# Optimization experiments

Measured on AMD Instinct MI355X. Metric: run time of the kernel, lower is better.

## Reference

```python
import jax, jax.numpy as jnp
import numpy as np

H, D, E, C, F = 12, 64, 768, 512, 3072  # heads, kq_dim, emb_dim, context_dim, mlp_hid
EPS = 1e-5
SCALE = 1.0 / float(np.sqrt(D))


def setup_inputs() -> dict:
    key = jax.random.key(0)
    ks = jax.random.split(key, 12)
    rn = lambda k, s: jax.random.normal(k, s, dtype=jnp.float32) * 0.02
    z = lambda s: jnp.zeros(s, jnp.float32)
    o = lambda s: jnp.ones(s, jnp.float32)
    return {
        "emb": jax.random.normal(ks[0], (8, 1024, E), dtype=jnp.float32),
        "context": jax.random.normal(ks[1], (8, 256, C), dtype=jnp.float32),
        # self-attention (qkv_bias=False, value_up has bias)
        "sa_wq": rn(ks[2], (E, H * D)), "sa_wk": rn(ks[3], (E, H * D)),
        "sa_wv": rn(ks[4], (E, H * D)), "sa_wo": rn(ks[5], (H * D, E)), "sa_wo_b": z((E,)),
        "sa_qn_g": o((D,)), "sa_qn_b": z((D,)), "sa_kn_g": o((D,)), "sa_kn_b": z((D,)),
        # cross-attention
        "ca_wq": rn(ks[6], (E, H * D)), "ca_wk": rn(ks[7], (C, H * D)),
        "ca_wv": rn(ks[8], (C, H * D)), "ca_wo": rn(ks[9], (H * D, E)), "ca_wo_b": z((E,)),
        "ca_qn_g": o((D,)), "ca_qn_b": z((D,)), "ca_kn_g": o((D,)), "ca_kn_b": z((D,)),
        # MLP
        "mlp_w1": rn(ks[10], (E, F)), "mlp_b1": z((F,)),
        "mlp_w2": rn(ks[11], (F, E)), "mlp_b2": z((E,)),
        # block LayerNorms
        "ln1_g": o((E,)), "ln1_b": z((E,)),
        "ln2_g": o((E,)), "ln2_b": z((E,)),
        "ln3_g": o((E,)), "ln3_b": z((E,)),
    }


def _ln(x, g, b):
    m = jnp.mean(x, axis=-1, keepdims=True)
    v = jnp.mean(jnp.square(x - m), axis=-1, keepdims=True)
    return (x - m) / jnp.sqrt(v + EPS) * g + b


def _heads(x):  # [B,S,H*D] -> [B,H,S,D]
    B, S = x.shape[:2]
    return x.reshape(B, S, H, D).transpose(0, 2, 1, 3)


def _merge(x):  # [B,H,S,D] -> [B,S,H*D]
    B, h, S, d = x.shape
    return x.transpose(0, 2, 1, 3).reshape(B, S, h * d)


def _attn(qx, kvx, wq, wk, wv, wo, wo_b, qg, qb, kg, kb):
    q = _ln(_heads(qx @ wq), qg, qb)   # per-head QK-LayerNorm
    k = _ln(_heads(kvx @ wk), kg, kb)
    v = _heads(kvx @ wv)
    a = jax.nn.softmax(jnp.einsum('bhqd,bhkd->bhqk', q, k) * SCALE, axis=-1)
    return _merge(jnp.einsum('bhqk,bhkd->bhqd', a, v)) @ wo + wo_b


def reference(emb, context,
              sa_wq, sa_wk, sa_wv, sa_wo, sa_wo_b, sa_qn_g, sa_qn_b, sa_kn_g, sa_kn_b,
              ca_wq, ca_wk, ca_wv, ca_wo, ca_wo_b, ca_qn_g, ca_qn_b, ca_kn_g, ca_kn_b,
              mlp_w1, mlp_b1, mlp_w2, mlp_b2,
              ln1_g, ln1_b, ln2_g, ln2_b, ln3_g, ln3_b):
    # MultiHeadAttention.forward returns value + emb, and the block adds emb again
    sa = _attn(emb, emb, sa_wq, sa_wk, sa_wv, sa_wo, sa_wo_b,
               sa_qn_g, sa_qn_b, sa_kn_g, sa_kn_b)
    x = _ln(sa + emb + emb, ln1_g, ln1_b)  # faithful double residual
    ca = _attn(x, context, ca_wq, ca_wk, ca_wv, ca_wo, ca_wo_b,
               ca_qn_g, ca_qn_b, ca_kn_g, ca_kn_b)
    x = _ln(x + ca, ln2_g, ln2_b)
    x = jax.nn.gelu(x @ mlp_w1 + mlp_b1, approximate=False) @ mlp_w2 + mlp_b2
    return _ln(x, ln3_g, ln3_b)  # note: no residual around MLP in the original
```

## Files before the change

kernel.cpp:

```cpp
#include <hip/hip_runtime.h>
#include <hip/hip_bf16.h>
#include <math.h>

#define NH 12
#define HD 64
#define ED 768
#define CD 512
#define FD 3072
#define BB 8
#define SS 1024
#define TT 256
#define LN_EPS 1e-5f
#define ATT_SCALE 0.125f
#define QSC_LOG2E 0.1803368801111204f
#define P_M0 11.55f
#define TOT_R 6291456

typedef __attribute__((ext_vector_type(8))) __bf16 bf16x8;
typedef __attribute__((ext_vector_type(4))) __bf16 bf16x4;
typedef __attribute__((ext_vector_type(4))) float f32x4;

typedef const __attribute__((address_space(1))) void* gas1_t;
typedef __attribute__((address_space(3))) void* las3_t;

__device__ __forceinline__ void gl16(const void* g, void* l) {
  __builtin_amdgcn_global_load_lds((gas1_t)g, (las3_t)l, 16, 0, 0);
}

__device__ __forceinline__ ushort f2bf(float f) {
  union { __bf16 b; ushort u; } c;
  c.b = (__bf16)f;
  return c.u;
}

__device__ __forceinline__ float gelu_fast(float c) {
  const float x2 = c * c;
  const float ex = __builtin_amdgcn_exp2f(c * (-2.3022084f - 0.10294325f * x2));
  return c * __builtin_amdgcn_rcpf(1.0f + ex);
}

__device__ __forceinline__ bf16x8 frag64(const ushort (*T)[64], int row, int q8) {
  return *(const bf16x8*)((const char*)T + row * 128 + ((q8 ^ (row & 7)) << 4));
}

__device__ __forceinline__ bf16x8 frag32(const ushort (*T)[32], int row, int g) {
  return *(const bf16x8*)((const char*)T + row * 64 + ((g ^ ((row >> 1) & 3)) << 4));
}

struct CvtPack {
  const float* src[12];
  ushort* dst[12];
  int kd[12];
  int nd[12];
  int off[13];
};

__global__ __launch_bounds__(256) void cvt_all(CvtPack P) {
  __shared__ float t[32][33];
  const int flat = blockIdx.x;
  int j = 0;
  while (j < 11 && flat >= P.off[j + 1]) ++j;
  const int rel = flat - P.off[j];
  if (P.nd[j] == 0) {
    const int i = rel * 256 + threadIdx.x;
    if (i < P.kd[j]) {
      float4 v = ((const float4*)P.src[j])[i];
      ((ushort4*)P.dst[j])[i] =
          make_ushort4(f2bf(v.x), f2bf(v.y), f2bf(v.z), f2bf(v.w));
    }
    return;
  }
  const int Kd = P.kd[j], Nd = P.nd[j];
  const int ntx = Nd >> 5;
  const int n0 = (rel % ntx) * 32, k0 = (rel / ntx) * 32;
  const float* W = P.src[j];
  ushort* WT = P.dst[j];
  const int tx = threadIdx.x & 31, ty = threadIdx.x >> 5;
#pragma unroll
  for (int r = 0; r < 4; ++r)
    t[ty + 8 * r][tx] = W[(size_t)(k0 + ty + 8 * r) * Nd + n0 + tx];
  __syncthreads();
#pragma unroll
  for (int r = 0; r < 4; ++r)
    WT[(size_t)(n0 + ty + 8 * r) * Kd + k0 + tx] = f2bf(t[tx][ty + 8 * r]);
}

template <int MODE, int BM>
__global__ __launch_bounds__(256, 3) void mfma_gemm(
    const ushort* __restrict__ A, const ushort* __restrict__ Wt,
    const float* __restrict__ bias, void* __restrict__ outp,
    int M, int N, int K, int sshift,
    const float* __restrict__ qg, const float* __restrict__ qb,
    const float* __restrict__ kg, const float* __restrict__ kb,
    int t_q, int t_k, int t_v) {
  constexpr int MI = BM / 32;
  __shared__ ushort As[2][BM][32];
  __shared__ ushort Bs[2][128][32];
  const int tid = threadIdx.x;
  const int m0 = blockIdx.x * BM, n0 = blockIdx.y * 128;
  const int lane = tid & 63;
  const int wr = ((tid >> 6) >> 1) * (BM / 2), wc = ((tid >> 6) & 1) * 64;
  const int l15 = lane & 15, g = lane >> 4;
  f32x4 acc[MI][4] = {};

  auto stage = [&](int bi, int kt) {
#pragma unroll
    for (int p = 0; p < BM / 64; ++p) {
      const int fq = p * 256 + tid;
      const int row = fq >> 2, q = fq & 3;
      const int kc = 8 * (q ^ ((row >> 1) & 3));
      gl16(&A[(size_t)(m0 + row) * K + kt + kc], (char*)As[bi] + fq * 16);
    }
#pragma unroll
    for (int p = 0; p < 2; ++p) {
      const int fq = p * 256 + tid;
      const int row = fq >> 2, q = fq & 3;
      const int kc = 8 * (q ^ ((row >> 1) & 3));
      gl16(&Wt[(size_t)(n0 + row) * K + kt + kc], (char*)Bs[bi] + fq * 16);
    }
  };

  stage(0, 0);
  __syncthreads();
  int cur = 0;
  for (int kt = 0; kt < K; kt += 32) {
    if (kt + 32 < K) stage(cur ^ 1, kt + 32);
    bf16x8 af[MI], bfv[4];
#pragma unroll
    for (int i = 0; i < MI; ++i) af[i] = frag32(As[cur], wr + i * 16 + l15, g);
#pragma unroll
    for (int j = 0; j < 4; ++j) bfv[j] = frag32(Bs[cur], wc + j * 16 + l15, g);
#pragma unroll
    for (int i = 0; i < MI; ++i)
#pragma unroll
      for (int j = 0; j < 4; ++j)
        acc[i][j] = __builtin_amdgcn_mfma_f32_16x16x32_bf16(af[i], bfv[j],
                                                            acc[i][j], 0, 0, 0);
    __syncthreads();
    cur ^= 1;
  }

  if (MODE == 2) {
    ushort* out = (ushort*)outp;
    const int Stok = 1 << sshift, smask = Stok - 1;
    const int ht0 = (n0 + wc) >> 6;
    const int t = ht0 / NH, h = ht0 - t * NH;
    const bool isq = (t == t_q), isk = (t == t_k);
    if (isq || isk) {
      const float* gg = isq ? qg : kg;
      const float* bb = isq ? qb : kb;
      const float osc = isq ? QSC_LOG2E : 1.0f;
      float gv[4], bv[4];
#pragma unroll
      for (int j = 0; j < 4; ++j) {
        gv[j] = gg[j * 16 + l15];
        bv[j] = bb[j * 16 + l15];
      }
#pragma unroll
      for (int i = 0; i < MI; ++i)
#pragma unroll
        for (int r = 0; r < 4; ++r) {
          float s = acc[i][0][r] + acc[i][1][r] + acc[i][2][r] + acc[i][3][r];
          float sq = acc[i][0][r] * acc[i][0][r] + acc[i][1][r] * acc[i][1][r] +
                     acc[i][2][r] * acc[i][2][r] + acc[i][3][r] * acc[i][3][r];
          s += __shfl_xor(s, 1);  sq += __shfl_xor(sq, 1);
          s += __shfl_xor(s, 2);  sq += __shfl_xor(sq, 2);
          s += __shfl_xor(s, 4);  sq += __shfl_xor(sq, 4);
          s += __shfl_xor(s, 8);  sq += __shfl_xor(sq, 8);
          const float mean = s * (1.0f / 64.0f);
          const float var = sq * (1.0f / 64.0f) - mean * mean;
          const float rs = rsqrtf(fmaxf(var, 0.0f) + LN_EPS);
#pragma unroll
          for (int j = 0; j < 4; ++j)
            acc[i][j][r] = ((acc[i][j][r] - mean) * rs * gv[j] + bv[j]) * osc;
        }
    }
    if (t == t_v) {
#pragma unroll
      for (int i = 0; i < MI; ++i) {
        const int row = m0 + wr + i * 16 + g * 4;
        const int b = row >> sshift, s2 = row & smask;
        ushort* obase =
            out + (size_t)t * TOT_R + (((size_t)b * NH + h) * 64) * Stok + s2;
#pragma unroll
        for (int j = 0; j < 4; ++j) {
          const int d = j * 16 + l15;
          ushort4 pk = make_ushort4(f2bf(acc[i][j][0]), f2bf(acc[i][j][1]),
                                    f2bf(acc[i][j][2]), f2bf(acc[i][j][3]));
          *(ushort4*)&obase[(size_t)d * Stok] = pk;
        }
      }
    } else {
#pragma unroll
      for (int i = 0; i < MI; ++i)
#pragma unroll
        for (int r = 0; r < 4; ++r) {
          const int row = m0 + wr + i * 16 + g * 4 + r;
          const int b = row >> sshift, s2 = row & smask;
          ushort* orow =
              out + (size_t)t * TOT_R + (((size_t)b * NH + h) * Stok + s2) * 64;
#pragma unroll
          for (int j = 0; j < 4; ++j) orow[j * 16 + l15] = f2bf(acc[i][j][r]);
        }
    }
  } else {
#pragma unroll
    for (int i = 0; i < MI; ++i) {
#pragma unroll
      for (int j = 0; j < 4; ++j) {
        const int gc = n0 + wc + j * 16 + l15;
        const float bv = bias ? bias[gc] : 0.0f;
#pragma unroll
        for (int r = 0; r < 4; ++r) {
          const int row = m0 + wr + i * 16 + g * 4 + r;
          float c = acc[i][j][r] + bv;
          if (MODE == 1) {
            c = gelu_fast(c);
            ((ushort*)outp)[(size_t)row * N + gc] = f2bf(c);
          } else {
            ((float*)outp)[(size_t)row * N + gc] = c;
          }
        }
      }
    }
  }
}

__global__ __launch_bounds__(512) void flash_mfma(
    const ushort* __restrict__ Q, const ushort* __restrict__ K,
    const ushort* __restrict__ V, ushort* __restrict__ out, int Tkv) {
  __shared__ ushort Ks[2][64][64];
  __shared__ ushort Vt[2][80][64];
  __shared__ ushort Ps[8][16][64];
  const int bh = blockIdx.x;
  const int b = bh / NH, h = bh % NH;
  const int qt = blockIdx.y;
  const int tid = threadIdx.x;
  const int w = tid >> 6, lane = tid & 63;
  const int l15 = lane & 15, g = lane >> 4;
  const int srow = tid >> 3;
  const int q8s = tid & 7;
  const int skc = 8 * (q8s ^ (srow & 7));
  const int kperm = 4 * (srow & 15) + (srow >> 4);

  const ushort* Qb = Q + ((size_t)bh * SS + qt * 256) * 64;
  const ushort* Kb = K + (size_t)bh * Tkv * 64;
  const ushort* Vb = V + (size_t)bh * Tkv * 64;

  gl16(&Kb[(size_t)kperm * 64 + skc], (char*)Ks[0] + tid * 16);
  gl16(&Vb[(size_t)srow * Tkv + skc], (char*)Vt[0] + tid * 16);

  if (tid < 256) {
    const int bi = tid >> 7, rq = tid & 127;
    const uint4 ov = make_uint4(0x3F803F80u, 0x3F803F80u, 0x3F803F80u, 0x3F803F80u);
    *(uint4*)((char*)Vt[bi] + (64 + (rq >> 3)) * 128 + ((rq & 7) << 4)) = ov;
  }

  const ushort* qr0 = Qb + (w * 32 + l15) * 64;
  const bf16x8 qf00 = *(const bf16x8*)&qr0[g * 8];
  const bf16x8 qf01 = *(const bf16x8*)&qr0[32 + g * 8];
  const bf16x8 qf10 = *(const bf16x8*)&qr0[16 * 64 + g * 8];
  const bf16x8 qf11 = *(const bf16x8*)&qr0[16 * 64 + 32 + g * 8];
  __syncthreads();

  f32x4 oa[2][5] = {};
  const int pwofs = ((((l15 >> 1) ^ ((g * 4) & 7)) << 4) | ((l15 & 1) << 3));

  const int nch = Tkv >> 6;
  int cur = 0;
  for (int ci = 0; ci < nch; ++ci) {
    if (ci + 1 < nch) {
      const int cnx = (ci + 1) << 6;
      const int nxt = cur ^ 1;
      gl16(&Kb[(size_t)(cnx + kperm) * 64 + skc], (char*)Ks[nxt] + tid * 16);
      gl16(&Vb[(size_t)srow * Tkv + cnx + skc], (char*)Vt[nxt] + tid * 16);
    }

    f32x4 s[2][4] = {};
    __builtin_amdgcn_s_setprio(1);
#pragma unroll
    for (int kb = 0; kb < 4; ++kb) {
      bf16x8 kf0 = frag64(Ks[cur], kb * 16 + l15, g);
      bf16x8 kf1 = frag64(Ks[cur], kb * 16 + l15, 4 + g);
      s[0][kb] = __builtin_amdgcn_mfma_f32_16x16x32_bf16(qf00, kf0, s[0][kb], 0, 0, 0);
      s[0][kb] = __builtin_amdgcn_mfma_f32_16x16x32_bf16(qf01, kf1, s[0][kb], 0, 0, 0);
      s[1][kb] = __builtin_amdgcn_mfma_f32_16x16x32_bf16(qf10, kf0, s[1][kb], 0, 0, 0);
      s[1][kb] = __builtin_amdgcn_mfma_f32_16x16x32_bf16(qf11, kf1, s[1][kb], 0, 0, 0);
    }
    __builtin_amdgcn_s_setprio(0);

    bf16x8 pfr[2][2];
#pragma unroll
    for (int sub = 0; sub < 2; ++sub) {
#pragma unroll
      for (int r = 0; r < 4; ++r) {
        bf16x4 pk;
#pragma unroll
        for (int kbv = 0; kbv < 4; ++kbv)
          pk[kbv] = (__bf16)__builtin_amdgcn_exp2f(s[sub][kbv][r] - P_M0);
        *(bf16x4*)((char*)Ps[w] + (g * 4 + r) * 128 + (pwofs ^ ((r & 7) << 4))) = pk;
      }
      pfr[sub][0] = frag64(Ps[w], l15, g);
      pfr[sub][1] = frag64(Ps[w], l15, 4 + g);
    }

    __builtin_amdgcn_s_setprio(1);
#pragma unroll
    for (int jd = 0; jd < 5; ++jd) {
      const int d = jd * 16 + l15;
      bf16x8 vf0 = frag64(Vt[cur], d, g);
      bf16x8 vf1 = frag64(Vt[cur], d, 4 + g);
      oa[0][jd] = __builtin_amdgcn_mfma_f32_16x16x32_bf16(pfr[0][0], vf0, oa[0][jd], 0, 0, 0);
      oa[0][jd] = __builtin_amdgcn_mfma_f32_16x16x32_bf16(pfr[0][1], vf1, oa[0][jd], 0, 0, 0);
      oa[1][jd] = __builtin_amdgcn_mfma_f32_16x16x32_bf16(pfr[1][0], vf0, oa[1][jd], 0, 0, 0);
      oa[1][jd] = __builtin_amdgcn_mfma_f32_16x16x32_bf16(pfr[1][1], vf1, oa[1][jd], 0, 0, 0);
    }
    __builtin_amdgcn_s_setprio(0);

    __syncthreads();
    cur ^= 1;
  }

#pragma unroll
  for (int sub = 0; sub < 2; ++sub)
#pragma unroll
    for (int r = 0; r < 4; ++r) {
      const int row = qt * 256 + w * 32 + sub * 16 + g * 4 + r;
      const float inv = 1.0f / oa[sub][4][r];
#pragma unroll
      for (int jd = 0; jd < 4; ++jd)
        out[((size_t)b * SS + row) * ED + h * 64 + jd * 16 + l15] =
            f2bf(oa[sub][jd][r] * inv);
    }
}

__global__ __launch_bounds__(256) void add_ln(
    const float* __restrict__ a, const float* __restrict__ bsrc, float alpha,
    const float* __restrict__ g, const float* __restrict__ bt,
    float* __restrict__ outf, ushort* __restrict__ outb) {
  const int row = blockIdx.x * 4 + (threadIdx.x >> 6);
  const int lane = threadIdx.x & 63;
  const size_t base = (size_t)row * ED;
  float4 x[3];
#pragma unroll
  for (int p = 0; p < 3; ++p) {
    const int idx = p * 256 + lane * 4;
    x[p] = *(const float4*)&a[base + idx];
    if (bsrc) {
      float4 bv = *(const float4*)&bsrc[base + idx];
      x[p].x += alpha * bv.x;
      x[p].y += alpha * bv.y;
      x[p].z += alpha * bv.z;
      x[p].w += alpha * bv.w;
    }
  }
  float s = 0.f;
#pragma unroll
  for (int p = 0; p < 3; ++p) s += x[p].x + x[p].y + x[p].z + x[p].w;
  for (int off = 32; off; off >>= 1) s += __shfl_xor(s, off);
  const float mean = s * (1.0f / 768.0f);
  float v = 0.f;
#pragma unroll
  for (int p = 0; p < 3; ++p) {
    float d0 = x[p].x - mean, d1 = x[p].y - mean;
    float d2 = x[p].z - mean, d3 = x[p].w - mean;
    v += d0 * d0 + d1 * d1 + d2 * d2 + d3 * d3;
  }
  for (int off = 32; off; off >>= 1) v += __shfl_xor(v, off);
  const float rs = rsqrtf(v * (1.0f / 768.0f) + LN_EPS);
#pragma unroll
  for (int p = 0; p < 3; ++p) {
    const int idx = p * 256 + lane * 4;
    const float4 gv = *(const float4*)&g[idx];
    const float4 bb = *(const float4*)&bt[idx];
    const float y0 = (x[p].x - mean) * rs * gv.x + bb.x;
    const float y1 = (x[p].y - mean) * rs * gv.y + bb.y;
    const float y2 = (x[p].z - mean) * rs * gv.z + bb.z;
    const float y3 = (x[p].w - mean) * rs * gv.w + bb.w;
    if (outf) *(float4*)&outf[base + idx] = make_float4(y0, y1, y2, y3);
    if (outb)
      *(ushort4*)&outb[base + idx] =
          make_ushort4(f2bf(y0), f2bf(y1), f2bf(y2), f2bf(y3));
  }
}

extern "C" void kernel_launch(void* const* d_in, const int* in_sizes, int n_in,
                              void* d_out, int out_size, void* d_ws,
                              size_t ws_size, hipStream_t stream) {
  (void)in_sizes; (void)n_in; (void)out_size; (void)ws_size;
  const float* emb     = (const float*)d_in[0];
  const float* context = (const float*)d_in[1];
  const float* sa_wq = (const float*)d_in[2];
  const float* sa_wk = (const float*)d_in[3];
  const float* sa_wv = (const float*)d_in[4];
  const float* sa_wo = (const float*)d_in[5];
  const float* sa_wo_b = (const float*)d_in[6];
  const float* sa_qn_g = (const float*)d_in[7];
  const float* sa_qn_b = (const float*)d_in[8];
  const float* sa_kn_g = (const float*)d_in[9];
  const float* sa_kn_b = (const float*)d_in[10];
  const float* ca_wq = (const float*)d_in[11];
  const float* ca_wk = (const float*)d_in[12];
  const float* ca_wv = (const float*)d_in[13];
  const float* ca_wo = (const float*)d_in[14];
  const float* ca_wo_b = (const float*)d_in[15];
  const float* ca_qn_g = (const float*)d_in[16];
  const float* ca_qn_b = (const float*)d_in[17];
  const float* ca_kn_g = (const float*)d_in[18];
  const float* ca_kn_b = (const float*)d_in[19];
  const float* mlp_w1 = (const float*)d_in[20];
  const float* mlp_b1 = (const float*)d_in[21];
  const float* mlp_w2 = (const float*)d_in[22];
  const float* mlp_b2 = (const float*)d_in[23];
  const float* ln1_g = (const float*)d_in[24];
  const float* ln1_b = (const float*)d_in[25];
  const float* ln2_g = (const float*)d_in[26];
  const float* ln2_b = (const float*)d_in[27];
  const float* ln3_g = (const float*)d_in[28];
  const float* ln3_b = (const float*)d_in[29];
  float* out = (float*)d_out;

  const size_t R = TOT_R;
  ushort* U = (ushort*)d_ws;
  ushort* Qh  = U;
  ushort* Kh  = U + R;
  ushort* Vh  = U + 2 * R;
  ushort* SH1 = U + 3 * R;
  ushort* SH2 = U + 4 * R;
  ushort* WB  = U + 5 * R;
  float*  X1  = (float*)(U + 5 * R + 9043968);
  float*  WOt = (float*)Qh;
  ushort* Hb  = Qh;

  ushort* w_saqkv = WB;
  ushort* w_sao   = WB + 1769472;
  ushort* w_caq   = WB + 2359296;
  ushort* w_cakv  = WB + 2949120;
  ushort* w_cao   = WB + 3735552;
  ushort* w_m1    = WB + 4325376;
  ushort* w_m2    = WB + 6684672;

  dim3 blk(256);

  CvtPack P;
  const float* srcs[12] = {sa_wq, sa_wk, sa_wv, sa_wo, ca_wq, ca_wk, ca_wv,
                           ca_wo, mlp_w1, mlp_w2, emb, context};
  ushort* dsts[12] = {w_saqkv, w_saqkv + 589824, w_saqkv + 1179648, w_sao,
                      w_caq, w_cakv, w_cakv + 393216, w_cao, w_m1, w_m2,
                      SH1, SH2};
  const int kds[12] = {ED, ED, ED, ED, ED, CD, CD, ED, ED, FD,
                       1572864, 262144};
  const int nds[12] = {ED, ED, ED, ED, ED, ED, ED, ED, FD, ED, 0, 0};
  int off = 0;
  for (int j = 0; j < 12; ++j) {
    P.src[j] = srcs[j]; P.dst[j] = dsts[j]; P.kd[j] = kds[j]; P.nd[j] = nds[j];
    P.off[j] = off;
    off += nds[j] ? (nds[j] >> 5) * (kds[j] >> 5) : (kds[j] + 255) >> 8;
  }
  P.off[12] = off;
  cvt_all<<<dim3(off), blk, 0, stream>>>(P);

  mfma_gemm<2, 128><<<dim3(64, 18), blk, 0, stream>>>(
      SH1, w_saqkv, nullptr, Qh, 8192, 2304, ED, 10,
      sa_qn_g, sa_qn_b, sa_kn_g, sa_kn_b, 0, 1, 2);
  flash_mfma<<<dim3(96, 4), dim3(512), 0, stream>>>(Qh, Kh, Vh, SH1, SS);
  mfma_gemm<0, 64><<<dim3(128, 6), blk, 0, stream>>>(
      SH1, w_sao, sa_wo_b, X1, 8192, ED, ED, 0,
      nullptr, nullptr, nullptr, nullptr, -1, -1, -1);
  add_ln<<<dim3(2048), blk, 0, stream>>>(X1, emb, 2.0f, ln1_g, ln1_b, X1, SH1);

  mfma_gemm<2, 64><<<dim3(128, 6), blk, 0, stream>>>(
      SH1, w_caq, nullptr, Qh, 8192, ED, ED, 10,
      ca_qn_g, ca_qn_b, nullptr, nullptr, 0, -1, -1);
  mfma_gemm<2, 64><<<dim3(32, 12), blk, 0, stream>>>(
      SH2, w_cakv, nullptr, Kh, 2048, 1536, CD, 8,
      nullptr, nullptr, ca_kn_g, ca_kn_b, -1, 0, 1);
  flash_mfma<<<dim3(96, 4), dim3(512), 0, stream>>>(Qh, Kh, Vh, SH1, TT);
  mfma_gemm<0, 64><<<dim3(128, 6), blk, 0, stream>>>(
      SH1, w_cao, ca_wo_b, WOt, 8192, ED, ED, 0,
      nullptr, nullptr, nullptr, nullptr, -1, -1, -1);
  add_ln<<<dim3(2048), blk, 0, stream>>>(WOt, X1, 1.0f, ln2_g, ln2_b, nullptr, SH2);

  mfma_gemm<1, 128><<<dim3(64, 24), blk, 0, stream>>>(
      SH2, w_m1, mlp_b1, Hb, 8192, FD, ED, 0,
      nullptr, nullptr, nullptr, nullptr, -1, -1, -1);
  mfma_gemm<0, 64><<<dim3(128, 6), blk, 0, stream>>>(
      Hb, w_m2, mlp_b2, X1, 8192, ED, FD, 0,
      nullptr, nullptr, nullptr, nullptr, -1, -1, -1);
  add_ln<<<dim3(2048), blk, 0, stream>>>(X1, nullptr, 0.0f, ln3_g, ln3_b, out,
                                         nullptr);
}
```

Baseline: 349.5 us.

## Split-K the N=768 GEMMs with larger tiles and fold partials and bias into LayerNorm

The three output-projection and MLP-down GEMMs (N=768) move from BM=64 tiles over the full K to BM=128 tiles with K split into two halves along grid z. Each half writes its own fp32 partial buffer, and add_ln now sums both partials plus the GEMM bias before the residual and normalisation. The cross-attention Q projection also moves to BM=128. The aim is more operand reuse per block at the same block count, at the cost of an extra fp32 partial write and read per row and a workspace region placed after X1.

```diff
diff --git a/kernel.cpp b/kernel.cpp
--- a/kernel.cpp
+++ b/kernel.cpp
@@ -89,7 +89,7 @@
 __global__ __launch_bounds__(256, 3) void mfma_gemm(
     const ushort* __restrict__ A, const ushort* __restrict__ Wt,
     const float* __restrict__ bias, void* __restrict__ outp,
-    int M, int N, int K, int sshift,
+    void* __restrict__ outp2, int M, int N, int Kstride, int Klen, int sshift,
     const float* __restrict__ qg, const float* __restrict__ qb,
     const float* __restrict__ kg, const float* __restrict__ kb,
     int t_q, int t_k, int t_v) {
@@ -98,6 +98,10 @@
   __shared__ ushort Bs[2][128][32];
   const int tid = threadIdx.x;
   const int m0 = blockIdx.x * BM, n0 = blockIdx.y * 128;
+  const int kz = blockIdx.z;
+  const ushort* Ab = A + (size_t)kz * Klen;
+  const ushort* Wb = Wt + (size_t)kz * Klen;
+  void* op = kz ? outp2 : outp;
   const int lane = tid & 63;
   const int wr = ((tid >> 6) >> 1) * (BM / 2), wc = ((tid >> 6) & 1) * 64;
   const int l15 = lane & 15, g = lane >> 4;
@@ -109,22 +113,22 @@
       const int fq = p * 256 + tid;
       const int row = fq >> 2, q = fq & 3;
       const int kc = 8 * (q ^ ((row >> 1) & 3));
-      gl16(&A[(size_t)(m0 + row) * K + kt + kc], (char*)As[bi] + fq * 16);
+      gl16(&Ab[(size_t)(m0 + row) * Kstride + kt + kc], (char*)As[bi] + fq * 16);
     }
 #pragma unroll
     for (int p = 0; p < 2; ++p) {
       const int fq = p * 256 + tid;
       const int row = fq >> 2, q = fq & 3;
       const int kc = 8 * (q ^ ((row >> 1) & 3));
-      gl16(&Wt[(size_t)(n0 + row) * K + kt + kc], (char*)Bs[bi] + fq * 16);
+      gl16(&Wb[(size_t)(n0 + row) * Kstride + kt + kc], (char*)Bs[bi] + fq * 16);
     }
   };
 
   stage(0, 0);
   __syncthreads();
   int cur = 0;
-  for (int kt = 0; kt < K; kt += 32) {
-    if (kt + 32 < K) stage(cur ^ 1, kt + 32);
+  for (int kt = 0; kt < Klen; kt += 32) {
+    if (kt + 32 < Klen) stage(cur ^ 1, kt + 32);
     bf16x8 af[MI], bfv[4];
 #pragma unroll
     for (int i = 0; i < MI; ++i) af[i] = frag32(As[cur], wr + i * 16 + l15, g);
@@ -141,7 +145,7 @@
   }
 
   if (MODE == 2) {
-    ushort* out = (ushort*)outp;
+    ushort* out = (ushort*)op;
     const int Stok = 1 << sshift, smask = Stok - 1;
     const int ht0 = (n0 + wc) >> 6;
     const int t = ht0 / NH, h = ht0 - t * NH;
@@ -216,9 +220,9 @@
           float c = acc[i][j][r] + bv;
           if (MODE == 1) {
             c = gelu_fast(c);
-            ((ushort*)outp)[(size_t)row * N + gc] = f2bf(c);
+            ((ushort*)op)[(size_t)row * N + gc] = f2bf(c);
           } else {
-            ((float*)outp)[(size_t)row * N + gc] = c;
+            ((float*)op)[(size_t)row * N + gc] = c;
           }
         }
       }
@@ -335,7 +339,9 @@
 }
 
 __global__ __launch_bounds__(256) void add_ln(
-    const float* __restrict__ a, const float* __restrict__ bsrc, float alpha,
+    const float* __restrict__ a1, const float* __restrict__ a2,
+    const float* __restrict__ bsrc, float alpha,
+    const float* __restrict__ cbias,
     const float* __restrict__ g, const float* __restrict__ bt,
     float* __restrict__ outf, ushort* __restrict__ outb) {
   const int row = blockIdx.x * 4 + (threadIdx.x >> 6);
@@ -345,13 +351,21 @@
 #pragma unroll
   for (int p = 0; p < 3; ++p) {
     const int idx = p * 256 + lane * 4;
-    x[p] = *(const float4*)&a[base + idx];
+    x[p] = *(const float4*)&a1[base + idx];
+    if (a2) {
+      float4 v = *(const float4*)&a2[base + idx];
+      x[p].x += v.x; x[p].y += v.y; x[p].z += v.z; x[p].w += v.w;
+    }
     if (bsrc) {
       float4 bv = *(const float4*)&bsrc[base + idx];
       x[p].x += alpha * bv.x;
       x[p].y += alpha * bv.y;
       x[p].z += alpha * bv.z;
       x[p].w += alpha * bv.w;
+    }
+    if (cbias) {
+      float4 cv = *(const float4*)&cbias[idx];
+      x[p].x += cv.x; x[p].y += cv.y; x[p].z += cv.z; x[p].w += cv.w;
     }
   }
   float s = 0.f;
@@ -429,6 +443,7 @@
   ushort* SH2 = U + 4 * R;
   ushort* WB  = U + 5 * R;
   float*  X1  = (float*)(U + 5 * R + 9043968);
+  float*  P2  = X1 + R;
   float*  WOt = (float*)Qh;
   ushort* Hb  = Qh;
 
@@ -460,33 +475,35 @@
   P.off[12] = off;
   cvt_all<<<dim3(off), blk, 0, stream>>>(P);
 
-  mfma_gemm<2, 128><<<dim3(64, 18), blk, 0, stream>>>(
-      SH1, w_saqkv, nullptr, Qh, 8192, 2304, ED, 10,
+  mfma_gemm<2, 128><<<dim3(64, 18, 1), blk, 0, stream>>>(
+      SH1, w_saqkv, nullptr, Qh, nullptr, 8192, 2304, ED, ED, 10,
       sa_qn_g, sa_qn_b, sa_kn_g, sa_kn_b, 0, 1, 2);
   flash_mfma<<<dim3(96, 4), dim3(512), 0, stream>>>(Qh, Kh, Vh, SH1, SS);
-  mfma_gemm<0, 64><<<dim3(128, 6), blk, 0, stream>>>(
-      SH1, w_sao, sa_wo_b, X1, 8192, ED, ED, 0,
+  mfma_gemm<0, 128><<<dim3(64, 6, 2), blk, 0, stream>>>(
+      SH1, w_sao, nullptr, X1, P2, 8192, ED, ED, ED / 2, 0,
       nullptr, nullptr, nullptr, nullptr, -1, -1, -1);
-  add_ln<<<dim3(2048), blk, 0, stream>>>(X1, emb, 2.0f, ln1_g, ln1_b, X1, SH1);
-
-  mfma_gemm<2, 64><<<dim3(128, 6), blk, 0, stream>>>(
-      SH1, w_caq, nullptr, Qh, 8192, ED, ED, 10,
+  add_ln<<<dim3(2048), blk, 0, stream>>>(X1, P2, emb, 2.0f, sa_wo_b,
+                                         ln1_g, ln1_b, X1, SH1);
+
+  mfma_gemm<2, 128><<<dim3(64, 6, 1), blk, 0, stream>>>(
+      SH1, w_caq, nullptr, Qh, nullptr, 8192, ED, ED, ED, 10,
       ca_qn_g, ca_qn_b, nullptr, nullptr, 0, -1, -1);
-  mfma_gemm<2, 64><<<dim3(32, 12), blk, 0, stream>>>(
-      SH2, w_cakv, nullptr, Kh, 2048, 1536, CD, 8,
+  mfma_gemm<2, 64><<<dim3(32, 12, 1), blk, 0, stream>>>(
+      SH2, w_cakv, nullptr, Kh, nullptr, 2048, 1536, CD, CD, 8,
       nullptr, nullptr, ca_kn_g, ca_kn_b, -1, 0, 1);
   flash_mfma<<<dim3(96, 4), dim3(512), 0, stream>>>(Qh, Kh, Vh, SH1, TT);
-  mfma_gemm<0, 64><<<dim3(128, 6), blk, 0, stream>>>(
-      SH1, w_cao, ca_wo_b, WOt, 8192, ED, ED, 0,
+  mfma_gemm<0, 128><<<dim3(64, 6, 2), blk, 0, stream>>>(
+      SH1, w_cao, nullptr, WOt, P2, 8192, ED, ED, ED / 2, 0,
       nullptr, nullptr, nullptr, nullptr, -1, -1, -1);
-  add_ln<<<dim3(2048), blk, 0, stream>>>(WOt, X1, 1.0f, ln2_g, ln2_b, nullptr, SH2);
-
-  mfma_gemm<1, 128><<<dim3(64, 24), blk, 0, stream>>>(
-      SH2, w_m1, mlp_b1, Hb, 8192, FD, ED, 0,
+  add_ln<<<dim3(2048), blk, 0, stream>>>(WOt, P2, X1, 1.0f, ca_wo_b,
+                                         ln2_g, ln2_b, nullptr, SH2);
+
+  mfma_gemm<1, 128><<<dim3(64, 24, 1), blk, 0, stream>>>(
+      SH2, w_m1, mlp_b1, Hb, nullptr, 8192, FD, ED, ED, 0,
       nullptr, nullptr, nullptr, nullptr, -1, -1, -1);
-  mfma_gemm<0, 64><<<dim3(128, 6), blk, 0, stream>>>(
-      Hb, w_m2, mlp_b2, X1, 8192, ED, FD, 0,
+  mfma_gemm<0, 128><<<dim3(64, 6, 2), blk, 0, stream>>>(
+      Hb, w_m2, nullptr, X1, P2, 8192, ED, FD, FD / 2, 0,
       nullptr, nullptr, nullptr, nullptr, -1, -1, -1);
-  add_ln<<<dim3(2048), blk, 0, stream>>>(X1, nullptr, 0.0f, ln3_g, ln3_b, out,
-                                         nullptr);
-}
+  add_ln<<<dim3(2048), blk, 0, stream>>>(X1, P2, nullptr, 0.0f, mlp_b2,
+                                         ln3_g, ln3_b, out, nullptr);
+}
```

After: 349.3 us. Within noise of the previous version (-0.1%).
